# Kernel tuning notes

Measured on AMD Instinct MI355X. Metric: run time of the kernel, lower is better.

Reference implementation:

```python
import jax, jax.numpy as jnp
import numpy as np

B, S, D, H = 2, 2048, 512, 8
DK = D // H

def setup_inputs() -> dict:
    key = jax.random.key(0)
    ks = jax.random.split(key, 13)
    inp = {
        'query': jax.random.normal(ks[0], (B, S, D), jnp.float32),
        'key': jax.random.normal(ks[1], (B, S, D), jnp.float32),
        'value': jax.random.normal(ks[2], (B, S, D), jnp.float32),
        'group_prob': jax.random.uniform(ks[3], (B, S, S), jnp.float32),
        'mask': jax.random.randint(ks[4], (B, S, S), 0, 2, jnp.int32),
        'Wq': jax.random.normal(ks[5], (D, D), jnp.float32) * 0.02,
        'bq': jax.random.normal(ks[6], (D,), jnp.float32) * 0.02,
        'Wk': jax.random.normal(ks[7], (D, D), jnp.float32) * 0.02,
        'bk': jax.random.normal(ks[8], (D,), jnp.float32) * 0.02,
        'Wv': jax.random.normal(ks[9], (D, D), jnp.float32) * 0.02,
        'bv': jax.random.normal(ks[10], (D,), jnp.float32) * 0.02,
        'Wo': jax.random.normal(ks[11], (D, D), jnp.float32) * 0.02,
        'bo': jax.random.normal(ks[12], (D,), jnp.float32) * 0.02,
    }
    return inp

def reference(query, key, value, group_prob, mask, Wq, bq, Wk, bk, Wv, bv, Wo, bo):
    # project and split heads: [B,S,D] -> [B,H,S,dk]
    def proj(x, W, b):
        return (x @ W.T + b).reshape(B, S, H, DK).transpose(0, 2, 1, 3)
    q = proj(query, Wq, bq)
    k = proj(key, Wk, bk)
    v = proj(value, Wv, bv)
    scale = 1.0 / np.sqrt(DK).astype(np.float32)
    scores = jnp.einsum('bhqd,bhkd->bhqk', q, k) * scale  # [B,H,S,S]
    # allowed = mask | identity-diagonal; disallowed positions get -1e9
    diag = jnp.eye(S, dtype=bool)
    allowed = (mask.astype(bool) | diag)[:, None, :, :]  # [B,1,S,S]
    scores = jnp.where(allowed, scores, jnp.float32(-1e9))
    p_attn = jax.nn.softmax(scores, axis=-1) * group_prob[:, None, :, :]
    # dropout is identity in eval/deterministic mode
    x = jnp.einsum('bhqk,bhkd->bhqd', p_attn, v)  # [B,H,S,dk]
    x = x.transpose(0, 2, 1, 3).reshape(B, S, D)
    return x @ Wo.T + bo
```

## Files before the change

kernel.cpp:

```cpp
#include <hip/hip_runtime.h>
#include <hip/hip_bf16.h>
#include <cstdint>
#include <cstddef>

typedef __attribute__((ext_vector_type(8))) short bf16x8;
typedef __attribute__((ext_vector_type(4))) float f32x4;
typedef __attribute__((address_space(3))) void lds_void;
typedef const __attribute__((address_space(1))) void g_void;

constexpr int Bc = 2, Sc = 2048, Dc = 512, Hc = 8, DKc = 64;
constexpr int SPLIT = 2;
constexpr int NKT = Sc / 64;
constexpr int KT_PER = NKT / SPLIT;
constexpr float CSC = 0.18033688011112042f;

struct alignas(16) us8 { unsigned short u[8]; };
struct alignas(8) us4 { unsigned short u[4]; };

__device__ __forceinline__ unsigned short f2bf(float x) {
  union { float f; unsigned int u; } v; v.f = x;
  unsigned int r = (v.u + 0x7FFFu + ((v.u >> 16) & 1u)) >> 16;
  return (unsigned short)r;
}

__device__ __forceinline__ float bf2f(unsigned short u) {
  union { unsigned int u; float f; } v; v.u = ((unsigned int)u) << 16;
  return v.f;
}

__device__ __forceinline__ us8 cvt8(float4 a, float4 b) {
  us8 o;
  o.u[0] = f2bf(a.x); o.u[1] = f2bf(a.y); o.u[2] = f2bf(a.z); o.u[3] = f2bf(a.w);
  o.u[4] = f2bf(b.x); o.u[5] = f2bf(b.y); o.u[6] = f2bf(b.z); o.u[7] = f2bf(b.w);
  return o;
}

struct WArgs { const float* wsrc[4]; unsigned short* wdst[4]; };

__global__ __launch_bounds__(256)
void prepass(const float* __restrict__ g, const int* __restrict__ m,
             unsigned short* __restrict__ gp, WArgs wa)
{
  __shared__ float Gs[64][64];
  __shared__ int   Ms[64][64];
  const int bx = blockIdx.x;
  const int tid = threadIdx.x;
  if (bx < 2048) {
    const int idx = bx;
    const int b = idx >> 10, rest = idx & 1023, qt = rest >> 5, kt = rest & 31;
    const int q0 = qt * 64, k0t = kt * 64;
    const int lane = tid & 63, w = tid >> 6;

#pragma unroll
    for (int i = 0; i < 4; ++i) {
      const int unit = w * 4 + i;
      const int row = unit * 4 + (lane >> 4);
      const int cbyte = ((lane & 15) * 16) ^ ((row & 7) << 4);
      const size_t sbase = ((size_t)(b * Sc + q0 + row)) * Sc + k0t + (cbyte >> 2);
      __builtin_amdgcn_global_load_lds((g_void*)(g + sbase), (lds_void*)((char*)&Gs[0][0] + unit * 1024), 16, 0, 0);
      __builtin_amdgcn_global_load_lds((g_void*)(m + sbase), (lds_void*)((char*)&Ms[0][0] + unit * 1024), 16, 0, 0);
    }
    asm volatile("s_waitcnt vmcnt(0)" ::: "memory");
    __syncthreads();

    const int colb = tid & 15, hi = (tid >> 4) & 3, wid = tid >> 6;
    const int qr = wid * 16 + colb;
    const int q = q0 + qr;
    char* gb = (char*)&Gs[0][0];
    char* mb = (char*)&Ms[0][0];
    unsigned short vals[16];
#pragma unroll
    for (int n = 0; n < 4; ++n) {
      const int addr = qr * 256 + ((n * 64 + hi * 16) ^ ((qr & 7) << 4));
      float4 gv = *(const float4*)(gb + addr);
      int4 mv = *(const int4*)(mb + addr);
      const int kb = k0t + n * 16 + hi * 4;
      const float gg[4] = {gv.x, gv.y, gv.z, gv.w};
      const int mm[4] = {mv.x, mv.y, mv.z, mv.w};
#pragma unroll
      for (int rr = 0; rr < 4; ++rr) {
        const bool allowed = (mm[rr] != 0) || (kb + rr == q);
        vals[n * 4 + rr] = allowed ? (unsigned short)(f2bf(gg[rr]) | 1u) : (unsigned short)0;
      }
    }
    us8* o = (us8*)(gp + (((size_t)idx * 256) + tid) * 16);
    o[0] = *(us8*)&vals[0];
    o[1] = *(us8*)&vals[8];
  } else {
    const int r = bx - 2048;
    const int wi = r >> 3, sub = r & 7;
    const float* s = wa.wsrc[wi];
    unsigned short* d = wa.wdst[wi];
#pragma unroll
    for (int t = 0; t < 16; ++t) {
      const int i = sub * 4096 + t * 256 + tid;
      float4 a = ((const float4*)s)[(size_t)i * 2];
      float4 b2 = ((const float4*)s)[(size_t)i * 2 + 1];
      ((us8*)d)[i] = cvt8(a, b2);
    }
  }
}

struct GArgs {
  const void* A[3];
  const unsigned short* W[3];
  const float* bias[3];
  void* C[3];
  int mode[3];
  float osc[3];
};

template<int A_FP32>
__global__ __launch_bounds__(256)
void gemm_bn64(GArgs ga)
{
  __shared__ unsigned short As[128][64];
  __shared__ unsigned short Bs[64][64];

  constexpr int K = 512, N = 512;
  const int z = blockIdx.z;
  const unsigned short* Wp = ga.W[z];
  const float* bias = ga.bias[z];
  const int mode = ga.mode[z];
  const float osc = ga.osc[z];

  const int tid = threadIdx.x, lane = tid & 63, w = tid >> 6;
  const int m0 = blockIdx.x * 128, n0 = blockIdx.y * 64;
  const int wm = w >> 1, wn = w & 1;
  const int colb = lane & 15, hi = lane >> 4, rowb = hi * 4;
  const int swz = (colb & 7) << 4;

  f32x4 acc[4][2];
#pragma unroll
  for (int i = 0; i < 4; ++i)
#pragma unroll
    for (int j = 0; j < 2; ++j) acc[i][j] = (f32x4){0.f, 0.f, 0.f, 0.f};

  const int lrow8 = lane >> 3;
  const int cb = ((lane & 7) * 16) ^ (lrow8 << 4);

  for (int k0 = 0; k0 < K; k0 += 64) {
    if (k0) __syncthreads();
#pragma unroll
    for (int i = 0; i < 2; ++i) {
      const int u = w + i * 4;
      const int row = u * 8 + lrow8;
      const unsigned short* bsrc = Wp + (size_t)(n0 + row) * K + k0 + (cb >> 1);
      __builtin_amdgcn_global_load_lds((g_void*)bsrc, (lds_void*)((char*)&Bs[0][0] + u * 1024), 16, 0, 0);
    }
    if (A_FP32) {
      const float* Af = (const float*)ga.A[z];
#pragma unroll
      for (int i = 0; i < 4; ++i) {
        const int u = w * 4 + i;
        const int row = u * 8 + lrow8;
        const float* src = Af + (size_t)(m0 + row) * K + k0 + (cb >> 1);
        float4 v0 = *(const float4*)src, v1 = *(const float4*)(src + 4);
        *(us8*)((char*)&As[0][0] + u * 1024 + lane * 16) = cvt8(v0, v1);
      }
    } else {
      const unsigned short* Ab = (const unsigned short*)ga.A[z];
#pragma unroll
      for (int i = 0; i < 4; ++i) {
        const int u = w * 4 + i;
        const int row = u * 8 + lrow8;
        const unsigned short* asrc = Ab + (size_t)(m0 + row) * K + k0 + (cb >> 1);
        __builtin_amdgcn_global_load_lds((g_void*)asrc, (lds_void*)((char*)&As[0][0] + u * 1024), 16, 0, 0);
      }
    }
    asm volatile("s_waitcnt vmcnt(0)" ::: "memory");
    __syncthreads();

    char* ab = (char*)&As[0][0];
    char* bb = (char*)&Bs[0][0];
#pragma unroll
    for (int kk = 0; kk < 2; ++kk) {
      bf16x8 af[4], bfr[2];
#pragma unroll
      for (int mf = 0; mf < 4; ++mf) {
        const int ar = wm * 64 + mf * 16 + colb;
        af[mf] = *(const bf16x8*)(ab + ar * 128 + ((kk * 64 + hi * 16) ^ swz));
      }
#pragma unroll
      for (int nf = 0; nf < 2; ++nf) {
        const int br = wn * 32 + nf * 16 + colb;
        bfr[nf] = *(const bf16x8*)(bb + br * 128 + ((kk * 64 + hi * 16) ^ swz));
      }
      __builtin_amdgcn_s_setprio(1);
#pragma unroll
      for (int mf = 0; mf < 4; ++mf)
#pragma unroll
        for (int nf = 0; nf < 2; ++nf)
          acc[mf][nf] = __builtin_amdgcn_mfma_f32_16x16x32_bf16(af[mf], bfr[nf], acc[mf][nf], 0, 0, 0);
      __builtin_amdgcn_s_setprio(0);
    }
  }

#pragma unroll
  for (int nf = 0; nf < 2; ++nf) {
    const int gn = n0 + wn * 32 + nf * 16 + colb;
    const float bv = bias[gn];
    if (mode == 1) {
      unsigned short* Cp = (unsigned short*)ga.C[z];
#pragma unroll
      for (int mf = 0; mf < 4; ++mf) {
        const int gm = m0 + wm * 64 + mf * 16 + rowb;
        const int bb_ = gm >> 11, ss = gm & (Sc - 1);
        us4 vv;
#pragma unroll
        for (int rr = 0; rr < 4; ++rr) vv.u[rr] = f2bf(acc[mf][nf][rr] + bv);
        *(us4*)(Cp + ((size_t)bb_ * N + gn) * Sc + ss) = vv;
      }
    } else if (mode == 0) {
      unsigned short* Cp = (unsigned short*)ga.C[z];
#pragma unroll
      for (int mf = 0; mf < 4; ++mf)
#pragma unroll
        for (int rr = 0; rr < 4; ++rr) {
          const int gm = m0 + wm * 64 + mf * 16 + rowb + rr;
          Cp[(size_t)gm * N + gn] = f2bf((acc[mf][nf][rr] + bv) * osc);
        }
    } else {
      float* Cp = (float*)ga.C[z];
#pragma unroll
      for (int mf = 0; mf < 4; ++mf)
#pragma unroll
        for (int rr = 0; rr < 4; ++rr) {
          const int gm = m0 + wm * 64 + mf * 16 + rowb + rr;
          Cp[(size_t)gm * N + gn] = acc[mf][nf][rr] + bv;
        }
    }
  }
}

__global__ __launch_bounds__(256, 4)
void attn_split(const unsigned short* __restrict__ Qb,
                const unsigned short* __restrict__ Kb,
                const unsigned short* __restrict__ Vt,
                const unsigned short* __restrict__ Gp,
                unsigned short* __restrict__ Pacc,
                float* __restrict__ Pml)
{
  __shared__ unsigned short Ks[2][64][64];
  __shared__ unsigned short Vs[2][64][64];
  __shared__ unsigned short Ps[4][16][64];

  const int tid = threadIdx.x, lane = tid & 63, wid = tid >> 6;
  const int wgid = blockIdx.x;
  const int xcd = wgid & 7, rest = wgid >> 3;
  const int mem = rest & 15, ghi = rest >> 4;
  const int g = ghi * 8 + xcd;
  const int b = g >> 5, qt = g & 31;
  const int h = mem >> 1, sp = mem & 1;
  const int bh = b * 8 + h;
  const int q0 = qt * 64;
  const int kt0 = sp * KT_PER;

  const int colb = lane & 15;
  const int hi = lane >> 4;
  const int rowb = hi * 4;
  const int c3s = (colb & 7) << 4;

  bf16x8 qf[2];
  {
    const unsigned short* qp = Qb + ((size_t)(b * Sc + q0 + wid * 16 + colb) * Dc + h * DKc + hi * 8);
    qf[0] = *(const bf16x8*)qp;
    qf[1] = *(const bf16x8*)(qp + 32);
  }

  f32x4 acc[4] = {{0,0,0,0},{0,0,0,0},{0,0,0,0},{0,0,0,0}};
  float lr0 = 0.f, lr1 = 0.f, lr2 = 0.f, lr3 = 0.f;

  auto stageKV = [&](int bufI, int kt) {
    const int k0 = kt * 64;
#pragma unroll
    for (int i = 0; i < 2; ++i) {
      const int obase = wid * 1024 + i * 4096;
      const int row = (obase >> 7) + (lane >> 3);
      const int cb = ((lane & 7) * 16) ^ ((row & 7) << 4);
      const unsigned short* ksrc = Kb + (size_t)(b * Sc + k0 + row) * Dc + h * DKc + (cb >> 1);
      const unsigned short* vsrc = Vt + ((size_t)b * Dc + h * DKc + row) * Sc + k0 + (cb >> 1);
      __builtin_amdgcn_global_load_lds((g_void*)ksrc, (lds_void*)((char*)&Ks[bufI][0][0] + obase), 16, 0, 0);
      __builtin_amdgcn_global_load_lds((g_void*)vsrc, (lds_void*)((char*)&Vs[bufI][0][0] + obase), 16, 0, 0);
    }
  };

  const unsigned short* gtile = Gp + (((size_t)(b * 1024 + qt * 32)) * 256 + tid) * 16;
  auto loadG = [&](int kt, us8& g0, us8& g1) {
    const us8* p = (const us8*)(gtile + (size_t)kt * 4096);
    g0 = p[0]; g1 = p[1];
  };

  us8 gA0, gA1, gB0, gB1;
  stageKV(0, kt0);
  loadG(kt0, gA0, gA1);
  asm volatile("s_waitcnt vmcnt(0)" ::: "memory");
  __syncthreads();

  char* psbase = (char*)&Ps[wid][0][0];

  auto doTile = [&](int kt, int bufI, us8& gc0, us8& gc1, us8& gn0, us8& gn1) {
    if (kt + 1 < kt0 + KT_PER) {
      stageKV(bufI ^ 1, kt + 1);
      loadG(kt + 1, gn0, gn1);
    }

    f32x4 sf[4] = {{0,0,0,0},{0,0,0,0},{0,0,0,0},{0,0,0,0}};
    char* ksb = (char*)&Ks[bufI][0][0];
    __builtin_amdgcn_s_setprio(1);
#pragma unroll
    for (int kk = 0; kk < 2; ++kk) {
#pragma unroll
      for (int n = 0; n < 4; ++n) {
        const int krow = n * 16 + colb;
        bf16x8 kf = *(const bf16x8*)(ksb + krow * 128 + ((kk * 64 + hi * 16) ^ ((krow & 7) << 4)));
        sf[n] = __builtin_amdgcn_mfma_f32_16x16x32_bf16(kf, qf[kk], sf[n], 0, 0, 0);
      }
    }
    __builtin_amdgcn_s_setprio(0);

    unsigned int pw[8];
#pragma unroll
    for (int n = 0; n < 4; ++n) {
      float lacc = 0.f;
#pragma unroll
      for (int s2 = 0; s2 < 2; ++s2) {
        const int jv = n * 4 + s2 * 2;
        const unsigned short u0 = (jv < 8) ? gc0.u[jv] : gc1.u[jv - 8];
        const unsigned short u1 = (jv + 1 < 8) ? gc0.u[jv + 1] : gc1.u[jv + 1 - 8];
        const float p0 = __builtin_amdgcn_exp2f(sf[n][s2 * 2]);
        const float p1 = __builtin_amdgcn_exp2f(sf[n][s2 * 2 + 1]);
        lacc = fmaf(p0, (float)(u0 & 1u), lacc);
        lacc = fmaf(p1, (float)(u1 & 1u), lacc);
        const float q0v = p0 * bf2f(u0), q1v = p1 * bf2f(u1);
        asm("v_cvt_pk_bf16_f32 %0, %1, %2" : "=v"(pw[n * 2 + s2]) : "v"(q0v), "v"(q1v));
      }
      if (n == 0) lr0 += lacc; else if (n == 1) lr1 += lacc;
      else if (n == 2) lr2 += lacc; else lr3 += lacc;
    }

#pragma unroll
    for (int n = 0; n < 4; ++n) {
      const unsigned long long w64 = ((unsigned long long)pw[n * 2 + 1] << 32) | pw[n * 2];
      *(unsigned long long*)(psbase + colb * 128 + ((n * 32 + hi * 8) ^ c3s)) = w64;
    }

    char* vsb = (char*)&Vs[bufI][0][0];
    __builtin_amdgcn_s_setprio(1);
#pragma unroll
    for (int kk = 0; kk < 2; ++kk) {
      bf16x8 pf = *(const bf16x8*)(psbase + colb * 128 + ((kk * 64 + hi * 16) ^ c3s));
#pragma unroll
      for (int n = 0; n < 4; ++n) {
        const int vrow = n * 16 + colb;
        bf16x8 vf = *(const bf16x8*)(vsb + vrow * 128 + ((kk * 64 + hi * 16) ^ ((vrow & 7) << 4)));
        acc[n] = __builtin_amdgcn_mfma_f32_16x16x32_bf16(vf, pf, acc[n], 0, 0, 0);
      }
    }
    __builtin_amdgcn_s_setprio(0);

    asm volatile("s_waitcnt vmcnt(0)" ::: "memory");
    __syncthreads();
  };

  for (int j = 0; j < KT_PER; j += 2) {
    doTile(kt0 + j,     0, gA0, gA1, gB0, gB1);
    doTile(kt0 + j + 1, 1, gB0, gB1, gA0, gA1);
  }

  float lrun = (lr0 + lr1) + (lr2 + lr3);
  lrun += __shfl_xor(lrun, 16);
  lrun += __shfl_xor(lrun, 32);

  const size_t blin = ((size_t)bh * 32 + qt) * SPLIT + sp;
  unsigned short* pa = Pacc + blin * 4096;
#pragma unroll
  for (int n = 0; n < 4; ++n)
#pragma unroll
    for (int rr = 0; rr < 4; ++rr)
      pa[(size_t)(n * 16 + rowb + rr) * 64 + wid * 16 + colb] = f2bf(acc[n][rr]);
  if (hi == 0) Pml[blin * 64 + wid * 16 + colb] = lrun;
}

__global__ __launch_bounds__(256)
void attn_reduce(const unsigned short* __restrict__ Pacc, const float* __restrict__ Pml,
                 unsigned short* __restrict__ Xb)
{
  const int gidx = blockIdx.x;
  const int bh = gidx >> 5, qt = gidx & 31;
  const int b = bh >> 3, h = bh & 7;
  const int tid = threadIdx.x;
  const int qi = tid & 63;
  const int d0 = (tid >> 6) * 16;
  const size_t pb = (size_t)gidx * SPLIT;

  float denom = 0.f;
#pragma unroll
  for (int s = 0; s < SPLIT; ++s) denom += Pml[(pb + s) * 64 + qi];
  const float inv = 1.0f / denom;

  unsigned short vals[16];
#pragma unroll
  for (int j = 0; j < 16; ++j) {
    float a = 0.f;
#pragma unroll
    for (int s = 0; s < SPLIT; ++s)
      a += bf2f(Pacc[(pb + s) * 4096 + (size_t)(d0 + j) * 64 + qi]);
    vals[j] = f2bf(a * inv);
  }
  unsigned short* xp = Xb + ((size_t)(b * Sc) + qt * 64 + qi) * Dc + h * DKc + d0;
  *(us8*)xp = *(us8*)&vals[0];
  *(us8*)(xp + 8) = *(us8*)&vals[8];
}

extern "C" void kernel_launch(void* const* d_in, const int* in_sizes, int n_in,
                              void* d_out, int out_size, void* d_ws, size_t ws_size,
                              hipStream_t stream)
{
  const float* query = (const float*)d_in[0];
  const float* key_  = (const float*)d_in[1];
  const float* value = (const float*)d_in[2];
  const float* gprob = (const float*)d_in[3];
  const int*   mask  = (const int*)d_in[4];
  const float* Wq = (const float*)d_in[5];
  const float* bq = (const float*)d_in[6];
  const float* Wk = (const float*)d_in[7];
  const float* bk = (const float*)d_in[8];
  const float* Wv = (const float*)d_in[9];
  const float* bv = (const float*)d_in[10];
  const float* Wo = (const float*)d_in[11];
  const float* bo = (const float*)d_in[12];
  float* out = (float*)d_out;

  const size_t elems = (size_t)Bc * Sc * Dc;
  const size_t gelems = (size_t)Bc * Sc * Sc;
  const size_t welems = (size_t)Dc * Dc;

  char* base = (char*)d_ws;
  unsigned short* Qb = (unsigned short*)(base);
  unsigned short* Kb = Qb + elems;
  unsigned short* Vt = Kb + elems;
  unsigned short* Xb = Vt + elems;
  unsigned short* Gp = Xb + elems;
  unsigned short* Wqb = Gp + gelems;
  unsigned short* Wkb = Wqb + welems;
  unsigned short* Wvb = Wkb + welems;
  unsigned short* Wob = Wvb + welems;
  unsigned short* Pacc = Wob + welems;
  float* Pml = (float*)(Pacc + (size_t)(Bc * Hc) * 32 * SPLIT * 4096);

  WArgs wa;
  wa.wsrc[0] = Wq; wa.wdst[0] = Wqb;
  wa.wsrc[1] = Wk; wa.wdst[1] = Wkb;
  wa.wsrc[2] = Wv; wa.wdst[2] = Wvb;
  wa.wsrc[3] = Wo; wa.wdst[3] = Wob;
  hipLaunchKernelGGL(prepass, dim3(2080), dim3(256), 0, stream, gprob, mask, Gp, wa);

  GArgs gq;
  gq.A[0] = (const void*)query; gq.W[0] = Wqb; gq.bias[0] = bq; gq.C[0] = (void*)Qb; gq.mode[0] = 0; gq.osc[0] = CSC;
  gq.A[1] = (const void*)key_;  gq.W[1] = Wkb; gq.bias[1] = bk; gq.C[1] = (void*)Kb; gq.mode[1] = 0; gq.osc[1] = 1.0f;
  gq.A[2] = (const void*)value; gq.W[2] = Wvb; gq.bias[2] = bv; gq.C[2] = (void*)Vt; gq.mode[2] = 1; gq.osc[2] = 1.0f;
  hipLaunchKernelGGL((gemm_bn64<1>), dim3(32, 8, 3), dim3(256), 0, stream, gq);

  hipLaunchKernelGGL(attn_split, dim3(1024), dim3(256), 0, stream, Qb, Kb, Vt, Gp, Pacc, Pml);
  hipLaunchKernelGGL(attn_reduce, dim3(Bc * Hc * 32), dim3(256), 0, stream, Pacc, Pml, Xb);

  GArgs go;
  go.A[0] = (const void*)Xb; go.W[0] = Wob; go.bias[0] = bo; go.C[0] = (void*)out; go.mode[0] = 2; go.osc[0] = 1.0f;
  go.A[1] = go.A[0]; go.W[1] = go.W[0]; go.bias[1] = go.bias[0]; go.C[1] = go.C[0]; go.mode[1] = 2; go.osc[1] = 1.0f;
  go.A[2] = go.A[0]; go.W[2] = go.W[0]; go.bias[2] = go.bias[0]; go.C[2] = go.C[0]; go.mode[2] = 2; go.osc[2] = 1.0f;
  hipLaunchKernelGGL((gemm_bn64<0>), dim3(32, 8, 1), dim3(256), 0, stream, go);
}
```

Before: 89.30 us.

## Fuse split-K attention reduction into output projection GEMM prologue

The separate attn_reduce kernel is removed. attn_split now writes each split's partial output in a row-major [B,S,D] layout, transposed through LDS with packed bf16 converts, plus per-row denominators. A new gemm_po kernel loads both partials, sums them, normalises them and converts to bf16 while filling its A tile, then runs the Wo projection. This saves one launch and the Xb write and read round trip, but the A-tile load becomes synchronous register loads plus conversion instead of async LDS loads, and each element is still rounded to bf16 twice.

```diff
diff --git a/kernel.cpp b/kernel.cpp
--- a/kernel.cpp
+++ b/kernel.cpp
@@ -233,12 +233,106 @@
   }
 }
 
+__global__ __launch_bounds__(256)
+void gemm_po(const unsigned short* __restrict__ P0, const unsigned short* __restrict__ P1,
+             const float* __restrict__ Lml, const unsigned short* __restrict__ Wp,
+             const float* __restrict__ bias, float* __restrict__ out)
+{
+  __shared__ unsigned short As[128][64];
+  __shared__ unsigned short Bs[64][64];
+
+  constexpr int K = 512, N = 512;
+  const int tid = threadIdx.x, lane = tid & 63, w = tid >> 6;
+  const int m0 = blockIdx.x * 128, n0 = blockIdx.y * 64;
+  const int wm = w >> 1, wn = w & 1;
+  const int colb = lane & 15, hi = lane >> 4, rowb = hi * 4;
+  const int swz = (colb & 7) << 4;
+
+  f32x4 acc[4][2];
+#pragma unroll
+  for (int i = 0; i < 4; ++i)
+#pragma unroll
+    for (int j = 0; j < 2; ++j) acc[i][j] = (f32x4){0.f, 0.f, 0.f, 0.f};
+
+  const int lrow8 = lane >> 3;
+  const int cb = ((lane & 7) * 16) ^ (lrow8 << 4);
+
+  for (int k0 = 0; k0 < K; k0 += 64) {
+    if (k0) __syncthreads();
+#pragma unroll
+    for (int i = 0; i < 2; ++i) {
+      const int u = w + i * 4;
+      const int row = u * 8 + lrow8;
+      const unsigned short* bsrc = Wp + (size_t)(n0 + row) * K + k0 + (cb >> 1);
+      __builtin_amdgcn_global_load_lds((g_void*)bsrc, (lds_void*)((char*)&Bs[0][0] + u * 1024), 16, 0, 0);
+    }
+    const int h = k0 >> 6;
+#pragma unroll
+    for (int i = 0; i < 4; ++i) {
+      const int u = w * 4 + i;
+      const int row = u * 8 + lrow8;
+      const int gm = m0 + row;
+      const int bb2 = gm >> 11, qq = gm & (Sc - 1);
+      const size_t off = (size_t)gm * K + k0 + (cb >> 1);
+      us8 p0 = *(const us8*)(P0 + off);
+      us8 p1 = *(const us8*)(P1 + off);
+      const float l0 = Lml[(size_t)(bb2 * 8 + h) * Sc + qq];
+      const float l1 = Lml[(size_t)(16 + bb2 * 8 + h) * Sc + qq];
+      const float inv = 1.0f / (l0 + l1);
+      us8 o;
+#pragma unroll
+      for (int j = 0; j < 8; ++j)
+        o.u[j] = f2bf((bf2f(p0.u[j]) + bf2f(p1.u[j])) * inv);
+      *(us8*)((char*)&As[0][0] + u * 1024 + lane * 16) = o;
+    }
+    asm volatile("s_waitcnt vmcnt(0)" ::: "memory");
+    __syncthreads();
+
+    char* ab = (char*)&As[0][0];
+    char* bb = (char*)&Bs[0][0];
+#pragma unroll
+    for (int kk = 0; kk < 2; ++kk) {
+      bf16x8 af[4], bfr[2];
+#pragma unroll
+      for (int mf = 0; mf < 4; ++mf) {
+        const int ar = wm * 64 + mf * 16 + colb;
+        af[mf] = *(const bf16x8*)(ab + ar * 128 + ((kk * 64 + hi * 16) ^ swz));
+      }
+#pragma unroll
+      for (int nf = 0; nf < 2; ++nf) {
+        const int br = wn * 32 + nf * 16 + colb;
+        bfr[nf] = *(const bf16x8*)(bb + br * 128 + ((kk * 64 + hi * 16) ^ swz));
+      }
+      __builtin_amdgcn_s_setprio(1);
+#pragma unroll
+      for (int mf = 0; mf < 4; ++mf)
+#pragma unroll
+        for (int nf = 0; nf < 2; ++nf)
+          acc[mf][nf] = __builtin_amdgcn_mfma_f32_16x16x32_bf16(af[mf], bfr[nf], acc[mf][nf], 0, 0, 0);
+      __builtin_amdgcn_s_setprio(0);
+    }
+  }
+
+#pragma unroll
+  for (int nf = 0; nf < 2; ++nf) {
+    const int gn = n0 + wn * 32 + nf * 16 + colb;
+    const float bv = bias[gn];
+#pragma unroll
+    for (int mf = 0; mf < 4; ++mf)
+#pragma unroll
+      for (int rr = 0; rr < 4; ++rr) {
+        const int gm = m0 + wm * 64 + mf * 16 + rowb + rr;
+        out[(size_t)gm * N + gn] = acc[mf][nf][rr] + bv;
+      }
+  }
+}
+
 __global__ __launch_bounds__(256, 4)
 void attn_split(const unsigned short* __restrict__ Qb,
                 const unsigned short* __restrict__ Kb,
                 const unsigned short* __restrict__ Vt,
                 const unsigned short* __restrict__ Gp,
-                unsigned short* __restrict__ Pacc,
+                unsigned short* __restrict__ Pout,
                 float* __restrict__ Pml)
 {
   __shared__ unsigned short Ks[2][64][64];
@@ -258,7 +352,6 @@
 
   const int colb = lane & 15;
   const int hi = lane >> 4;
-  const int rowb = hi * 4;
   const int c3s = (colb & 7) << 4;
 
   bf16x8 qf[2];
@@ -277,9 +370,9 @@
     for (int i = 0; i < 2; ++i) {
       const int obase = wid * 1024 + i * 4096;
       const int row = (obase >> 7) + (lane >> 3);
-      const int cb = ((lane & 7) * 16) ^ ((row & 7) << 4);
-      const unsigned short* ksrc = Kb + (size_t)(b * Sc + k0 + row) * Dc + h * DKc + (cb >> 1);
-      const unsigned short* vsrc = Vt + ((size_t)b * Dc + h * DKc + row) * Sc + k0 + (cb >> 1);
+      const int cbk = ((lane & 7) * 16) ^ ((row & 7) << 4);
+      const unsigned short* ksrc = Kb + (size_t)(b * Sc + k0 + row) * Dc + h * DKc + (cbk >> 1);
+      const unsigned short* vsrc = Vt + ((size_t)b * Dc + h * DKc + row) * Sc + k0 + (cbk >> 1);
       __builtin_amdgcn_global_load_lds((g_void*)ksrc, (lds_void*)((char*)&Ks[bufI][0][0] + obase), 16, 0, 0);
       __builtin_amdgcn_global_load_lds((g_void*)vsrc, (lds_void*)((char*)&Vs[bufI][0][0] + obase), 16, 0, 0);
     }
@@ -372,45 +465,24 @@
   lrun += __shfl_xor(lrun, 16);
   lrun += __shfl_xor(lrun, 32);
 
-  const size_t blin = ((size_t)bh * 32 + qt) * SPLIT + sp;
-  unsigned short* pa = Pacc + blin * 4096;
-#pragma unroll
-  for (int n = 0; n < 4; ++n)
-#pragma unroll
-    for (int rr = 0; rr < 4; ++rr)
-      pa[(size_t)(n * 16 + rowb + rr) * 64 + wid * 16 + colb] = f2bf(acc[n][rr]);
-  if (hi == 0) Pml[blin * 64 + wid * 16 + colb] = lrun;
-}
-
-__global__ __launch_bounds__(256)
-void attn_reduce(const unsigned short* __restrict__ Pacc, const float* __restrict__ Pml,
-                 unsigned short* __restrict__ Xb)
-{
-  const int gidx = blockIdx.x;
-  const int bh = gidx >> 5, qt = gidx & 31;
-  const int b = bh >> 3, h = bh & 7;
-  const int tid = threadIdx.x;
-  const int qi = tid & 63;
-  const int d0 = (tid >> 6) * 16;
-  const size_t pb = (size_t)gidx * SPLIT;
-
-  float denom = 0.f;
-#pragma unroll
-  for (int s = 0; s < SPLIT; ++s) denom += Pml[(pb + s) * 64 + qi];
-  const float inv = 1.0f / denom;
-
-  unsigned short vals[16];
-#pragma unroll
-  for (int j = 0; j < 16; ++j) {
-    float a = 0.f;
-#pragma unroll
-    for (int s = 0; s < SPLIT; ++s)
-      a += bf2f(Pacc[(pb + s) * 4096 + (size_t)(d0 + j) * 64 + qi]);
-    vals[j] = f2bf(a * inv);
-  }
-  unsigned short* xp = Xb + ((size_t)(b * Sc) + qt * 64 + qi) * Dc + h * DKc + d0;
-  *(us8*)xp = *(us8*)&vals[0];
-  *(us8*)(xp + 8) = *(us8*)&vals[8];
+#pragma unroll
+  for (int n = 0; n < 4; ++n) {
+    unsigned int pw0, pw1;
+    asm("v_cvt_pk_bf16_f32 %0, %1, %2" : "=v"(pw0) : "v"(acc[n][0]), "v"(acc[n][1]));
+    asm("v_cvt_pk_bf16_f32 %0, %1, %2" : "=v"(pw1) : "v"(acc[n][2]), "v"(acc[n][3]));
+    const unsigned long long w64 = ((unsigned long long)pw1 << 32) | pw0;
+    *(unsigned long long*)(psbase + colb * 128 + ((n * 32 + hi * 8) ^ c3s)) = w64;
+  }
+  const int qrow = lane >> 2;
+  const int dseg = (lane & 3) * 16;
+  const int qsw = (qrow & 7) << 4;
+  us8 o0 = *(const us8*)(psbase + qrow * 128 + ((dseg * 2) ^ qsw));
+  us8 o1 = *(const us8*)(psbase + qrow * 128 + ((dseg * 2 + 16) ^ qsw));
+  unsigned short* xp = Pout + (size_t)sp * ((size_t)Bc * Sc * Dc)
+                     + ((size_t)(b * Sc) + q0 + wid * 16 + qrow) * Dc + h * DKc + dseg;
+  *(us8*)xp = o0;
+  *(us8*)(xp + 8) = o1;
+  if (hi == 0) Pml[((size_t)sp * 16 + bh) * Sc + q0 + wid * 16 + colb] = lrun;
 }
 
 extern "C" void kernel_launch(void* const* d_in, const int* in_sizes, int n_in,
@@ -440,14 +512,13 @@
   unsigned short* Qb = (unsigned short*)(base);
   unsigned short* Kb = Qb + elems;
   unsigned short* Vt = Kb + elems;
-  unsigned short* Xb = Vt + elems;
-  unsigned short* Gp = Xb + elems;
-  unsigned short* Wqb = Gp + gelems;
+  unsigned short* Gp = Vt + elems;
+  unsigned short* Pout = Gp + gelems;
+  float* Pml = (float*)(Pout + 2 * elems);
+  unsigned short* Wqb = (unsigned short*)(Pml + 2 * 16 * Sc);
   unsigned short* Wkb = Wqb + welems;
   unsigned short* Wvb = Wkb + welems;
   unsigned short* Wob = Wvb + welems;
-  unsigned short* Pacc = Wob + welems;
-  float* Pml = (float*)(Pacc + (size_t)(Bc * Hc) * 32 * SPLIT * 4096);
 
   WArgs wa;
   wa.wsrc[0] = Wq; wa.wdst[0] = Wqb;
@@ -462,12 +533,8 @@
   gq.A[2] = (const void*)value; gq.W[2] = Wvb; gq.bias[2] = bv; gq.C[2] = (void*)Vt; gq.mode[2] = 1; gq.osc[2] = 1.0f;
   hipLaunchKernelGGL((gemm_bn64<1>), dim3(32, 8, 3), dim3(256), 0, stream, gq);
 
-  hipLaunchKernelGGL(attn_split, dim3(1024), dim3(256), 0, stream, Qb, Kb, Vt, Gp, Pacc, Pml);
-  hipLaunchKernelGGL(attn_reduce, dim3(Bc * Hc * 32), dim3(256), 0, stream, Pacc, Pml, Xb);
-
-  GArgs go;
-  go.A[0] = (const void*)Xb; go.W[0] = Wob; go.bias[0] = bo; go.C[0] = (void*)out; go.mode[0] = 2; go.osc[0] = 1.0f;
-  go.A[1] = go.A[0]; go.W[1] = go.W[0]; go.bias[1] = go.bias[0]; go.C[1] = go.C[0]; go.mode[1] = 2; go.osc[1] = 1.0f;
-  go.A[2] = go.A[0]; go.W[2] = go.W[0]; go.bias[2] = go.bias[0]; go.C[2] = go.C[0]; go.mode[2] = 2; go.osc[2] = 1.0f;
-  hipLaunchKernelGGL((gemm_bn64<0>), dim3(32, 8, 1), dim3(256), 0, stream, go);
-}
+  hipLaunchKernelGGL(attn_split, dim3(1024), dim3(256), 0, stream, Qb, Kb, Vt, Gp, Pout, Pml);
+
+  hipLaunchKernelGGL(gemm_po, dim3(32, 8), dim3(256), 0, stream,
+                     Pout, Pout + elems, Pml, Wob, bo, out);
+}
```

Measured after the change: 91.68 us. 2.7% more time.
